# Kernel optimization log

Measured on AMD Instinct MI355X. Metric: run time of the kernel, lower is better.

The kernel has to match this reference:

```python
import jax, jax.numpy as jnp
import numpy as np

N = 4
SEGMENTS = 16
IN_F = 256
OUT_F = 256
BATCH = 512


def chebyshev_lobatto(n):
    # Chebyshev-Lobatto interpolation nodes on [-1, 1]
    k = jnp.arange(n, dtype=jnp.float32)
    return -jnp.cos(jnp.pi * k / (n - 1))


def lagrange_basis(x, nodes):
    # x: [B, In]; returns basis values [B, In, n]
    n = nodes.shape[0]
    cols = []
    for j in range(n):  # n is a small static constant (4)
        terms = [(x - nodes[m]) / (nodes[j] - nodes[m]) for m in range(n) if m != j]
        cols.append(jnp.prod(jnp.stack(terms, axis=0), axis=0))
    return jnp.stack(cols, axis=-1)


def setup_inputs() -> dict:
    key = jax.random.key(0)
    k1, k2 = jax.random.split(key)
    x = jax.random.uniform(k1, (BATCH, IN_F), dtype=jnp.float32, minval=-1.0, maxval=1.0)
    w = jax.random.uniform(
        k2, (OUT_F, IN_F, (N - 1) * SEGMENTS + 1), dtype=jnp.float32, minval=-1.0, maxval=1.0
    )
    return {"x": x, "w": w, "n": N, "segments": SEGMENTS}


def reference(x, w, n, segments):
    nodes = chebyshev_lobatto(n)
    # segment id per element, clamped to [0, segments-1]
    id_min = jnp.clip(((x + 1.0) / 2.0 * segments).astype(jnp.int32), 0, segments - 1)
    id_max = id_min + 1
    wid_min = id_min * (n - 1)  # start of weight slice; slice length == n
    # segment boundaries in x-space: eta(i) = i/segments * 2 - 1
    x_min = id_min.astype(x.dtype) / segments * 2.0 - 1.0
    x_max = id_max.astype(x.dtype) / segments * 2.0 - 1.0
    # rescale x into [-1, 1] within its segment
    x_in = 2.0 * (x - x_min) / (x_max - x_min) - 1.0
    basis = lagrange_basis(x_in, nodes)  # [B, In, n]
    # gather per-element weight slice: w_g[b,i,j,o] = w[o, i, wid_min[b,i]+j]
    idx = wid_min[..., None] + jnp.arange(n)  # [B, In, n]
    w_t = jnp.transpose(w, (1, 2, 0))  # [In, K, Out]
    in_f = w.shape[1]
    w_g = w_t[jnp.arange(in_f)[None, :, None], idx]  # [B, In, n, Out]
    # interpolate and sum over in_features (matches einsum 'ijk,jkli->jl')
    return jnp.einsum("bin,bino->bo", basis, w_g)
```

## Files before the change

### kernel.cpp

```cpp
#include <hip/hip_runtime.h>


typedef _Float16 h2 __attribute__((ext_vector_type(2)));

#define INF     256
#define OUTF    256
#define WSTRIDE 49
#define OSTRIDE (INF * WSTRIDE)
#define NSPLIT  16
#define IPB     16
#define WE_UINTS (256 * 128 * 64)

#define GLOAD16(gptr, lptr)                                                         \
  __builtin_amdgcn_global_load_lds(                                                 \
      (const __attribute__((address_space(1))) unsigned int*)(gptr),                \
      (__attribute__((address_space(3))) unsigned int*)(lptr), 16, 0, 0)

__global__ __launch_bounds__(256)
void pp_expand(const float* __restrict__ w, unsigned int* __restrict__ we) {
    __shared__ float lds_w[2][3136];

    const int tid   = threadIdx.x;
    const int op    = blockIdx.x >> 1;
    const int ihalf = blockIdx.x & 1;
    const int o0    = op * 2;

    for (int c = 0; c < 2; ++c) {
        const int i_c = ihalf * 128 + c * 64;

        #pragma unroll
        for (int oe = 0; oe < 2; ++oe) {
            const float* src = w + (size_t)(o0 + oe) * OSTRIDE + (size_t)i_c * WSTRIDE;
            #pragma unroll
            for (int it = 0; it < 4; ++it) {
                int u = it * 256 + tid;
                if (u < 784)
                    GLOAD16(src + u * 4, &lds_w[oe][u * 4]);
            }
        }
        __syncthreads();

        #pragma unroll
        for (int r = 0; r < 4; ++r) {
            int item = r * 256 + tid;
            int il = item >> 4, s = item & 15;
            const float* t0 = &lds_w[0][il * 49 + 3 * s];
            const float* t1 = &lds_w[1][il * 49 + 3 * s];
            uint4 v;
            v.x = __builtin_bit_cast(unsigned int,
                      __builtin_amdgcn_cvt_pkrtz(t0[0], t0[1]));
            v.y = __builtin_bit_cast(unsigned int,
                      __builtin_amdgcn_cvt_pkrtz(t0[2], t0[3]));
            v.z = __builtin_bit_cast(unsigned int,
                      __builtin_amdgcn_cvt_pkrtz(t1[0], t1[1]));
            v.w = __builtin_bit_cast(unsigned int,
                      __builtin_amdgcn_cvt_pkrtz(t1[2], t1[3]));
            *(uint4*)(we + (((size_t)(i_c + il) * 128 + op) * 16 + s) * 4) = v;
        }
        __syncthreads();
    }
}

__global__ __launch_bounds__(512, 4)
void pp_partial(const float* __restrict__ x, const unsigned int* __restrict__ we,
                float* __restrict__ part) {
    __shared__ unsigned int smem[16384];

    const int tid  = threadIdx.x;
    const int wave = tid >> 6, lane = tid & 63;
    const int osub = wave & 3;
    const int bsub = wave >> 2;
    const int isplit  = blockIdx.x;
    const int i_base  = isplit * IPB;
    const int op_base = blockIdx.y * 16;
    const int o_base  = blockIdx.y * 32;
    const int b_base  = blockIdx.z * 128;
    const int b = b_base + bsub * 64 + lane;

    #pragma unroll
    for (int it = 0; it < 8; ++it) {
        int u = it * 512 + tid;
        int iloc = u >> 8, opl = (u >> 4) & 15, s = u & 15;
        const unsigned int* gp =
            we + (((size_t)(i_base + iloc) * 128 + op_base + opl) * 16 + s) * 4;
        GLOAD16(gp, &smem[u * 4]);
    }

    int sseg[IPB]; h2 cA[IPB], cB[IPB];
    {
        const float4* xp = (const float4*)(x + (size_t)b * INF + i_base);
        float4 x0 = xp[0], x1 = xp[1], x2 = xp[2], x3 = xp[3];
        float xs[16] = {x0.x, x0.y, x0.z, x0.w, x1.x, x1.y, x1.z, x1.w,
                        x2.x, x2.y, x2.z, x2.w, x3.x, x3.y, x3.z, x3.w};
        #pragma unroll
        for (int i = 0; i < IPB; ++i) {
            float xx = xs[i];
            int id = (int)((xx + 1.0f) * 8.0f);
            id = id < 0 ? 0 : (id > 15 ? 15 : id);
            float u = (xx - ((float)id * 0.125f - 1.0f)) * 16.0f - 1.0f;
            float a = u + 1.0f, b2 = u + 0.5f, cc = u - 0.5f, d = u - 1.0f;
            float c0 = b2 * cc * d  * (-2.0f / 3.0f);
            float c1 = a  * cc * d  * ( 4.0f / 3.0f);
            float c2 = a  * b2 * d  * (-4.0f / 3.0f);
            float c3 = a  * b2 * cc * ( 2.0f / 3.0f);
            h2 pA; pA[0] = (_Float16)c0; pA[1] = (_Float16)c1;
            h2 pB; pB[0] = (_Float16)c2; pB[1] = (_Float16)c3;
            cA[i] = pA; cB[i] = pB; sseg[i] = id;
        }
    }

    __syncthreads();

    float acc[8];
    #pragma unroll
    for (int q = 0; q < 8; ++q) acc[q] = 0.0f;

    #pragma unroll
    for (int i = 0; i < IPB; ++i) {
        const unsigned int* p = &smem[(i * 16 + osub * 4) * 64 + sseg[i] * 4];
        #pragma unroll
        for (int pq = 0; pq < 4; ++pq) {
            uint4 v = *(const uint4*)(p + pq * 64);
            acc[2*pq]   = __builtin_amdgcn_fdot2(__builtin_bit_cast(h2, v.x), cA[i],
                                                 acc[2*pq],   false);
            acc[2*pq]   = __builtin_amdgcn_fdot2(__builtin_bit_cast(h2, v.y), cB[i],
                                                 acc[2*pq],   false);
            acc[2*pq+1] = __builtin_amdgcn_fdot2(__builtin_bit_cast(h2, v.z), cA[i],
                                                 acc[2*pq+1], false);
            acc[2*pq+1] = __builtin_amdgcn_fdot2(__builtin_bit_cast(h2, v.w), cB[i],
                                                 acc[2*pq+1], false);
        }
    }

    __syncthreads();
    float* smf = (float*)smem;
    const int b_l0 = bsub * 64 + lane;
    #pragma unroll
    for (int q = 0; q < 8; ++q)
        smf[b_l0 * 33 + osub * 8 + q] = acc[q];
    __syncthreads();

    const int qo = tid & 7;
    const int g  = tid >> 3;
    #pragma unroll
    for (int r = 0; r < 2; ++r) {
        int b_l = g + 64 * r;
        float4 v;
        v.x = smf[b_l * 33 + qo * 4 + 0];
        v.y = smf[b_l * 33 + qo * 4 + 1];
        v.z = smf[b_l * 33 + qo * 4 + 2];
        v.w = smf[b_l * 33 + qo * 4 + 3];
        *(float4*)(part + (size_t)isplit * (512 * 256)
                        + (size_t)(b_base + b_l) * 256 + o_base + qo * 4) = v;
    }
}

__global__ __launch_bounds__(256)
void pp_reduce(const float* __restrict__ part, float* __restrict__ out) {
    const size_t off4 = (size_t)blockIdx.x * 256 + threadIdx.x;
    const float4* p4 = (const float4*)part;
    float4 s = make_float4(0.f, 0.f, 0.f, 0.f);
    #pragma unroll
    for (int k = 0; k < NSPLIT; ++k) {
        float4 v = p4[(size_t)k * (512 * 64) + off4];
        s.x += v.x; s.y += v.y; s.z += v.z; s.w += v.w;
    }
    ((float4*)out)[off4] = s;
}

extern "C" void kernel_launch(void* const* d_in, const int* in_sizes, int n_in,
                              void* d_out, int out_size, void* d_ws, size_t ws_size,
                              hipStream_t stream) {
    const float* x = (const float*)d_in[0];
    const float* w = (const float*)d_in[1];
    float* out = (float*)d_out;
    unsigned int* we = (unsigned int*)d_ws;
    float* part = (float*)((char*)d_ws + (size_t)WE_UINTS * 4);
    (void)ws_size; (void)n_in; (void)in_sizes; (void)out_size;

    pp_expand<<<dim3(256), 256, 0, stream>>>(w, we);
    pp_partial<<<dim3(NSPLIT, 8, 4), 512, 0, stream>>>(x, we, part);
    pp_reduce<<<dim3(128), 256, 0, stream>>>(part, out);
}
```

Measured before the change: 83.92 us.

## Split expand grid, pipeline LDS loads in partial, and widen reduce grid

pp_expand now covers its two i-chunks with a second grid dimension instead of a serial loop, giving 512 blocks rather than 256. pp_partial issues the x loads first, then the LDS-direct weight loads in two halves. It waits only for the first half (vmcnt(4)) before computing on the first 8 inputs, so the second half's transfer can overlap that compute. pp_reduce uses 256 blocks of 128 threads for more parallelism. The hand-written waitcnt and barrier sequence depends on exact load counts and compiler scheduling, so a miscount could cause a race.

```diff
diff --git a/kernel.cpp b/kernel.cpp
--- a/kernel.cpp
+++ b/kernel.cpp
@@ -23,41 +23,38 @@
     const int tid   = threadIdx.x;
     const int op    = blockIdx.x >> 1;
     const int ihalf = blockIdx.x & 1;
+    const int c     = blockIdx.y;
     const int o0    = op * 2;
-
-    for (int c = 0; c < 2; ++c) {
-        const int i_c = ihalf * 128 + c * 64;
-
-        #pragma unroll
-        for (int oe = 0; oe < 2; ++oe) {
-            const float* src = w + (size_t)(o0 + oe) * OSTRIDE + (size_t)i_c * WSTRIDE;
-            #pragma unroll
-            for (int it = 0; it < 4; ++it) {
-                int u = it * 256 + tid;
-                if (u < 784)
-                    GLOAD16(src + u * 4, &lds_w[oe][u * 4]);
-            }
-        }
-        __syncthreads();
-
-        #pragma unroll
-        for (int r = 0; r < 4; ++r) {
-            int item = r * 256 + tid;
-            int il = item >> 4, s = item & 15;
-            const float* t0 = &lds_w[0][il * 49 + 3 * s];
-            const float* t1 = &lds_w[1][il * 49 + 3 * s];
-            uint4 v;
-            v.x = __builtin_bit_cast(unsigned int,
-                      __builtin_amdgcn_cvt_pkrtz(t0[0], t0[1]));
-            v.y = __builtin_bit_cast(unsigned int,
-                      __builtin_amdgcn_cvt_pkrtz(t0[2], t0[3]));
-            v.z = __builtin_bit_cast(unsigned int,
-                      __builtin_amdgcn_cvt_pkrtz(t1[0], t1[1]));
-            v.w = __builtin_bit_cast(unsigned int,
-                      __builtin_amdgcn_cvt_pkrtz(t1[2], t1[3]));
-            *(uint4*)(we + (((size_t)(i_c + il) * 128 + op) * 16 + s) * 4) = v;
-        }
-        __syncthreads();
+    const int i_c   = ihalf * 128 + c * 64;
+
+    #pragma unroll
+    for (int oe = 0; oe < 2; ++oe) {
+        const float* src = w + (size_t)(o0 + oe) * OSTRIDE + (size_t)i_c * WSTRIDE;
+        #pragma unroll
+        for (int it = 0; it < 4; ++it) {
+            int u = it * 256 + tid;
+            if (u < 784)
+                GLOAD16(src + u * 4, &lds_w[oe][u * 4]);
+        }
+    }
+    __syncthreads();
+
+    #pragma unroll
+    for (int r = 0; r < 4; ++r) {
+        int item = r * 256 + tid;
+        int il = item >> 4, s = item & 15;
+        const float* t0 = &lds_w[0][il * 49 + 3 * s];
+        const float* t1 = &lds_w[1][il * 49 + 3 * s];
+        uint4 v;
+        v.x = __builtin_bit_cast(unsigned int,
+                  __builtin_amdgcn_cvt_pkrtz(t0[0], t0[1]));
+        v.y = __builtin_bit_cast(unsigned int,
+                  __builtin_amdgcn_cvt_pkrtz(t0[2], t0[3]));
+        v.z = __builtin_bit_cast(unsigned int,
+                  __builtin_amdgcn_cvt_pkrtz(t1[0], t1[1]));
+        v.w = __builtin_bit_cast(unsigned int,
+                  __builtin_amdgcn_cvt_pkrtz(t1[2], t1[3]));
+        *(uint4*)(we + (((size_t)(i_c + il) * 128 + op) * 16 + s) * 4) = v;
     }
 }
 
@@ -77,19 +74,31 @@
     const int b_base  = blockIdx.z * 128;
     const int b = b_base + bsub * 64 + lane;
 
-    #pragma unroll
-    for (int it = 0; it < 8; ++it) {
+    const float4* xp = (const float4*)(x + (size_t)b * INF + i_base);
+    float4 x0 = xp[0], x1 = xp[1], x2 = xp[2], x3 = xp[3];
+    __builtin_amdgcn_sched_barrier(0);
+
+    #pragma unroll
+    for (int it = 0; it < 4; ++it) {
         int u = it * 512 + tid;
         int iloc = u >> 8, opl = (u >> 4) & 15, s = u & 15;
         const unsigned int* gp =
             we + (((size_t)(i_base + iloc) * 128 + op_base + opl) * 16 + s) * 4;
         GLOAD16(gp, &smem[u * 4]);
     }
+    __builtin_amdgcn_sched_barrier(0);
+    #pragma unroll
+    for (int it = 4; it < 8; ++it) {
+        int u = it * 512 + tid;
+        int iloc = u >> 8, opl = (u >> 4) & 15, s = u & 15;
+        const unsigned int* gp =
+            we + (((size_t)(i_base + iloc) * 128 + op_base + opl) * 16 + s) * 4;
+        GLOAD16(gp, &smem[u * 4]);
+    }
+    __builtin_amdgcn_sched_barrier(0);
 
     int sseg[IPB]; h2 cA[IPB], cB[IPB];
     {
-        const float4* xp = (const float4*)(x + (size_t)b * INF + i_base);
-        float4 x0 = xp[0], x1 = xp[1], x2 = xp[2], x3 = xp[3];
         float xs[16] = {x0.x, x0.y, x0.z, x0.w, x1.x, x1.y, x1.z, x1.w,
                         x2.x, x2.y, x2.z, x2.w, x3.x, x3.y, x3.z, x3.w};
         #pragma unroll
@@ -109,14 +118,38 @@
         }
     }
 
-    __syncthreads();
-
     float acc[8];
     #pragma unroll
     for (int q = 0; q < 8; ++q) acc[q] = 0.0f;
 
-    #pragma unroll
-    for (int i = 0; i < IPB; ++i) {
+    asm volatile("s_waitcnt vmcnt(4)" ::: "memory");
+    __builtin_amdgcn_s_barrier();
+    __builtin_amdgcn_sched_barrier(0);
+
+    #pragma unroll
+    for (int i = 0; i < 8; ++i) {
+        const unsigned int* p = &smem[(i * 16 + osub * 4) * 64 + sseg[i] * 4];
+        #pragma unroll
+        for (int pq = 0; pq < 4; ++pq) {
+            uint4 v = *(const uint4*)(p + pq * 64);
+            acc[2*pq]   = __builtin_amdgcn_fdot2(__builtin_bit_cast(h2, v.x), cA[i],
+                                                 acc[2*pq],   false);
+            acc[2*pq]   = __builtin_amdgcn_fdot2(__builtin_bit_cast(h2, v.y), cB[i],
+                                                 acc[2*pq],   false);
+            acc[2*pq+1] = __builtin_amdgcn_fdot2(__builtin_bit_cast(h2, v.z), cA[i],
+                                                 acc[2*pq+1], false);
+            acc[2*pq+1] = __builtin_amdgcn_fdot2(__builtin_bit_cast(h2, v.w), cB[i],
+                                                 acc[2*pq+1], false);
+        }
+    }
+    __builtin_amdgcn_sched_barrier(0);
+
+    asm volatile("s_waitcnt vmcnt(0)" ::: "memory");
+    __builtin_amdgcn_s_barrier();
+    __builtin_amdgcn_sched_barrier(0);
+
+    #pragma unroll
+    for (int i = 8; i < 16; ++i) {
         const unsigned int* p = &smem[(i * 16 + osub * 4) * 64 + sseg[i] * 4];
         #pragma unroll
         for (int pq = 0; pq < 4; ++pq) {
@@ -155,9 +188,9 @@
     }
 }
 
-__global__ __launch_bounds__(256)
+__global__ __launch_bounds__(128)
 void pp_reduce(const float* __restrict__ part, float* __restrict__ out) {
-    const size_t off4 = (size_t)blockIdx.x * 256 + threadIdx.x;
+    const size_t off4 = (size_t)blockIdx.x * 128 + threadIdx.x;
     const float4* p4 = (const float4*)part;
     float4 s = make_float4(0.f, 0.f, 0.f, 0.f);
     #pragma unroll
@@ -178,7 +211,7 @@
     float* part = (float*)((char*)d_ws + (size_t)WE_UINTS * 4);
     (void)ws_size; (void)n_in; (void)in_sizes; (void)out_size;
 
-    pp_expand<<<dim3(256), 256, 0, stream>>>(w, we);
+    pp_expand<<<dim3(256, 2), 256, 0, stream>>>(w, we);
     pp_partial<<<dim3(NSPLIT, 8, 4), 512, 0, stream>>>(x, we, part);
-    pp_reduce<<<dim3(128), 256, 0, stream>>>(part, out);
-}
+    pp_reduce<<<dim3(256), 128, 0, stream>>>(part, out);
+}
```

Result: no change. 84.65 us (+0.9%).

## Fuse weight fp16 expansion into partial kernel, drop separate expand pass

Applied to the files above, without the earlier changes.

Removes the pp_expand kernel and its intermediate fp16 weight buffer. Each pp_partial block now reads its fp32 weight rows straight from the original layout, converts them to packed fp16 and writes the segment-major tile into LDS itself. This saves a kernel launch and a global round trip of the expanded weights. In exchange every one of the 4 batch-tile blocks re-reads and re-converts the same weights using strided scalar loads instead of async global-to-LDS copies. The reduce kernel is also relaunched with 128-thread blocks and twice as many blocks.

```diff
diff --git a/kernel.cpp b/kernel.cpp
--- a/kernel.cpp
+++ b/kernel.cpp
@@ -9,60 +9,9 @@
 #define OSTRIDE (INF * WSTRIDE)
 #define NSPLIT  16
 #define IPB     16
-#define WE_UINTS (256 * 128 * 64)
-
-#define GLOAD16(gptr, lptr)                                                         \
-  __builtin_amdgcn_global_load_lds(                                                 \
-      (const __attribute__((address_space(1))) unsigned int*)(gptr),                \
-      (__attribute__((address_space(3))) unsigned int*)(lptr), 16, 0, 0)
-
-__global__ __launch_bounds__(256)
-void pp_expand(const float* __restrict__ w, unsigned int* __restrict__ we) {
-    __shared__ float lds_w[2][3136];
-
-    const int tid   = threadIdx.x;
-    const int op    = blockIdx.x >> 1;
-    const int ihalf = blockIdx.x & 1;
-    const int o0    = op * 2;
-
-    for (int c = 0; c < 2; ++c) {
-        const int i_c = ihalf * 128 + c * 64;
-
-        #pragma unroll
-        for (int oe = 0; oe < 2; ++oe) {
-            const float* src = w + (size_t)(o0 + oe) * OSTRIDE + (size_t)i_c * WSTRIDE;
-            #pragma unroll
-            for (int it = 0; it < 4; ++it) {
-                int u = it * 256 + tid;
-                if (u < 784)
-                    GLOAD16(src + u * 4, &lds_w[oe][u * 4]);
-            }
-        }
-        __syncthreads();
-
-        #pragma unroll
-        for (int r = 0; r < 4; ++r) {
-            int item = r * 256 + tid;
-            int il = item >> 4, s = item & 15;
-            const float* t0 = &lds_w[0][il * 49 + 3 * s];
-            const float* t1 = &lds_w[1][il * 49 + 3 * s];
-            uint4 v;
-            v.x = __builtin_bit_cast(unsigned int,
-                      __builtin_amdgcn_cvt_pkrtz(t0[0], t0[1]));
-            v.y = __builtin_bit_cast(unsigned int,
-                      __builtin_amdgcn_cvt_pkrtz(t0[2], t0[3]));
-            v.z = __builtin_bit_cast(unsigned int,
-                      __builtin_amdgcn_cvt_pkrtz(t1[0], t1[1]));
-            v.w = __builtin_bit_cast(unsigned int,
-                      __builtin_amdgcn_cvt_pkrtz(t1[2], t1[3]));
-            *(uint4*)(we + (((size_t)(i_c + il) * 128 + op) * 16 + s) * 4) = v;
-        }
-        __syncthreads();
-    }
-}
 
 __global__ __launch_bounds__(512, 4)
-void pp_partial(const float* __restrict__ x, const unsigned int* __restrict__ we,
+void pp_partial(const float* __restrict__ x, const float* __restrict__ w,
                 float* __restrict__ part) {
     __shared__ unsigned int smem[16384];
 
@@ -72,24 +21,42 @@
     const int bsub = wave >> 2;
     const int isplit  = blockIdx.x;
     const int i_base  = isplit * IPB;
-    const int op_base = blockIdx.y * 16;
     const int o_base  = blockIdx.y * 32;
     const int b_base  = blockIdx.z * 128;
     const int b = b_base + bsub * 64 + lane;
 
-    #pragma unroll
-    for (int it = 0; it < 8; ++it) {
-        int u = it * 512 + tid;
-        int iloc = u >> 8, opl = (u >> 4) & 15, s = u & 15;
-        const unsigned int* gp =
-            we + (((size_t)(i_base + iloc) * 128 + op_base + opl) * 16 + s) * 4;
-        GLOAD16(gp, &smem[u * 4]);
+    const float4* xp = (const float4*)(x + (size_t)b * INF + i_base);
+    float4 x0 = xp[0], x1 = xp[1], x2 = xp[2], x3 = xp[3];
+
+    {
+        const int o_loc = tid >> 4;
+        const int il    = tid & 15;
+        const int opl   = o_loc >> 1;
+        const int e     = o_loc & 1;
+        const float* row = w + (size_t)(o_base + o_loc) * OSTRIDE
+                             + (size_t)(i_base + il) * WSTRIDE;
+        unsigned int* dst = &smem[((il * 16 + opl) * 16) * 4 + e * 2];
+
+        #pragma unroll
+        for (int h = 0; h < 2; ++h) {
+            const float* rp = row + 24 * h;
+            float f[25];
+            #pragma unroll
+            for (int k = 0; k < 25; ++k) f[k] = rp[k];
+            #pragma unroll
+            for (int u = 0; u < 8; ++u) {
+                auto p0 = __builtin_amdgcn_cvt_pkrtz(f[3*u],   f[3*u+1]);
+                auto p1 = __builtin_amdgcn_cvt_pkrtz(f[3*u+2], f[3*u+3]);
+                uint2 v;
+                v.x = __builtin_bit_cast(unsigned int, p0);
+                v.y = __builtin_bit_cast(unsigned int, p1);
+                *(uint2*)(dst + (h * 8 + u) * 4) = v;
+            }
+        }
     }
 
     int sseg[IPB]; h2 cA[IPB], cB[IPB];
     {
-        const float4* xp = (const float4*)(x + (size_t)b * INF + i_base);
-        float4 x0 = xp[0], x1 = xp[1], x2 = xp[2], x3 = xp[3];
         float xs[16] = {x0.x, x0.y, x0.z, x0.w, x1.x, x1.y, x1.z, x1.w,
                         x2.x, x2.y, x2.z, x2.w, x3.x, x3.y, x3.z, x3.w};
         #pragma unroll
@@ -155,9 +122,9 @@
     }
 }
 
-__global__ __launch_bounds__(256)
+__global__ __launch_bounds__(128)
 void pp_reduce(const float* __restrict__ part, float* __restrict__ out) {
-    const size_t off4 = (size_t)blockIdx.x * 256 + threadIdx.x;
+    const size_t off4 = (size_t)blockIdx.x * 128 + threadIdx.x;
     const float4* p4 = (const float4*)part;
     float4 s = make_float4(0.f, 0.f, 0.f, 0.f);
     #pragma unroll
@@ -174,11 +141,9 @@
     const float* x = (const float*)d_in[0];
     const float* w = (const float*)d_in[1];
     float* out = (float*)d_out;
-    unsigned int* we = (unsigned int*)d_ws;
-    float* part = (float*)((char*)d_ws + (size_t)WE_UINTS * 4);
+    float* part = (float*)d_ws;
     (void)ws_size; (void)n_in; (void)in_sizes; (void)out_size;
 
-    pp_expand<<<dim3(256), 256, 0, stream>>>(w, we);
-    pp_partial<<<dim3(NSPLIT, 8, 4), 512, 0, stream>>>(x, we, part);
-    pp_reduce<<<dim3(128), 256, 0, stream>>>(part, out);
+    pp_partial<<<dim3(NSPLIT, 8, 4), 512, 0, stream>>>(x, w, part);
+    pp_reduce<<<dim3(256), 128, 0, stream>>>(part, out);
 }
```

Result: no change. 83.58 us (-0.4%).
